# Kernel tuning notes

Hardware: AMD Instinct MI355X
Metric: run time of the kernel (lower is better)

Reference implementation:

```python
import jax, jax.numpy as jnp
import numpy as np

VOCAB = 32000
DIM = 1024
N_BLOCKS = 5
L_CONST = 1e9


def setup_inputs() -> dict:
    key = jax.random.key(0)
    k1, k2, k3, k4, k5, k6 = jax.random.split(key, 6)
    x = jax.random.normal(k1, (2, 2048, DIM), dtype=jnp.float32)
    gates_w = jax.random.uniform(k2, (VOCAB, 1), dtype=jnp.float32)  # mimics uniform_(0.001, 1.0)
    weight = jax.random.normal(k3, (DIM, VOCAB), dtype=jnp.float32) * 0.02
    bias = jax.random.normal(k4, (VOCAB,), dtype=jnp.float32) * 0.02
    blk_w = jax.random.normal(k5, (N_BLOCKS, DIM, DIM), dtype=jnp.float32) * 0.02
    blk_b = jax.random.normal(k6, (N_BLOCKS, DIM), dtype=jnp.float32) * 0.02
    return {"x": x, "gates_w": gates_w, "weight": weight, "bias": bias, "blk_w": blk_w, "blk_b": blk_b}


def reference(x, gates_w, weight, bias, blk_w, blk_b):
    input_dim, vocab = weight.shape  # [D, V]
    gates = gates_w * input_dim  # [V, 1], scaled per-token gate
    idx = jnp.arange(input_dim, dtype=jnp.float32)[None, :]  # [1, D]
    # discrete mask + straight-through residual term (broadcast [V,1] over [V,D])
    mask = (idx < gates).astype(jnp.float32) + (L_CONST * gates - jnp.floor(L_CONST * gates)) / L_CONST  # [V, D]
    masked_weight = weight * mask.T  # [D, V]
    # branch selector per vocab column, in {0,...,4}
    selector = jnp.floor(gates / x.shape[-1] * N_BLOCKS * (1.0 - 1e-10)).reshape(vocab)  # [V]
    ret = jnp.zeros(x.shape[:-1] + (vocab,), dtype=x.dtype)
    for bidx in range(N_BLOCKS):
        x_b = jnp.einsum('bsd,ed->bse', x, blk_w[bidx]) + blk_b[bidx]  # Linear: x @ W^T + b
        temp = jnp.einsum('bsd,dv->bsv', x_b, masked_weight)  # [B, S, V]
        ret = ret + temp * (selector == bidx).astype(jnp.float32)
    return ret + bias
```

## Files before the change

### kernel.cpp

```cpp
#include <hip/hip_runtime.h>
#include <hip/hip_bf16.h>

#define VOCAB 32000
#define DIM 1024
#define NTOK 4096
#define NG 5
#define MAXTILES 255
#define PW 32640

typedef float f32x4 __attribute__((ext_vector_type(4)));
typedef __bf16 bf16x8 __attribute__((ext_vector_type(8)));

__device__ __forceinline__ unsigned short f2bf(float f) {
    union { float f; unsigned int u; } x; x.f = f;
    unsigned int r = x.u + 0x7fffu + ((x.u >> 16) & 1u);
    return (unsigned short)(r >> 16);
}
__device__ __forceinline__ float bf2f(unsigned short u) {
    union { unsigned int u; float f; } x; x.u = ((unsigned int)u) << 16;
    return x.f;
}

__device__ __forceinline__ void gload16(const void* g, void* l) {
    __builtin_amdgcn_global_load_lds(
        (const __attribute__((address_space(1))) void*)g,
        (__attribute__((address_space(3))) void*)l, 16, 0, 0);
}

__global__ __launch_bounds__(256) void hist_kernel(const float* __restrict__ gates_w,
                                                   int* __restrict__ hist) {
    __shared__ int cnt[NG];
    const int tid = threadIdx.x;
    if (tid < NG) cnt[tid] = 0;
    __syncthreads();
    const int v = blockIdx.x * 256 + tid;
    const int s = min(4, max(0, (int)floorf(gates_w[v] * 5.0f)));
    atomicAdd(&cnt[s], 1);
    __syncthreads();
    if (tid < NG) hist[blockIdx.x * NG + tid] = cnt[tid];
}

__global__ __launch_bounds__(64) void base_kernel(const int* __restrict__ hist,
                                                  int* __restrict__ blkoff,
                                                  int* __restrict__ jlist,
                                                  int4* __restrict__ tdesc,
                                                  int* __restrict__ pbase6) {
    __shared__ int histl[125 * NG];
    __shared__ int cnt[NG], pb[NG], padc[NG];
    const int tid = threadIdx.x;
    for (int i = tid; i < 125 * NG; i += 64) histl[i] = hist[i];
    __syncthreads();
    if (tid == 0) {
        int c[NG] = {0, 0, 0, 0, 0};
        for (int b = 0; b < 125; ++b)
            for (int g = 0; g < NG; ++g) c[g] += histl[b * NG + g];
        const int kmaxs[NG] = {256, 448, 640, 832, 1024};
        int p = 0, t = 0;
        for (int g = 0; g < NG; ++g) {
            pb[g] = p; cnt[g] = c[g];
            padc[g] = ((c[g] + 127) >> 7) << 7;
            pbase6[g] = p;
            p += padc[g];
        }
        pbase6[NG] = p;
        for (int g = 0; g < NG; ++g) {
            int nt = (cnt[g] + 127) >> 7;
            for (int k = 0; k < nt; ++k) { tdesc[t] = make_int4(g, pb[g] + (k << 7), kmaxs[g], 0); ++t; }
        }
        for (; t < MAXTILES; ++t) tdesc[t] = make_int4(-1, 0, 0, 0);
        int run[NG];
        for (int g = 0; g < NG; ++g) run[g] = pb[g];
        for (int b = 0; b < 125; ++b)
            for (int g = 0; g < NG; ++g) { blkoff[b * NG + g] = run[g]; run[g] += histl[b * NG + g]; }
    }
    __syncthreads();
    for (int g = 0; g < NG; ++g)
        for (int i = pb[g] + cnt[g] + tid; i < pb[g] + padc[g]; i += 64) jlist[i] = -1;
}

__global__ __launch_bounds__(256) void place_kernel(const float* __restrict__ gates_w,
                                                    const int* __restrict__ blkoff,
                                                    int* __restrict__ pos,
                                                    int* __restrict__ jlist) {
    __shared__ int wtot[4][NG], wpre[4][NG];
    const int tid = threadIdx.x, lane = tid & 63, wv = tid >> 6;
    const int v = blockIdx.x * 256 + tid;
    const int s = min(4, max(0, (int)floorf(gates_w[v] * 5.0f)));
    int rank = 0;
#pragma unroll
    for (int g = 0; g < NG; ++g) {
        unsigned long long m = __ballot(s == g);
        if (lane == 0) wtot[wv][g] = (int)__popcll(m);
        if (s == g) rank = (int)__popcll(m & ((1ull << lane) - 1ull));
    }
    __syncthreads();
    if (tid < NG) {
        int a = 0;
        for (int w = 0; w < 4; ++w) { wpre[w][tid] = a; a += wtot[w][tid]; }
    }
    __syncthreads();
    const int p = blkoff[blockIdx.x * NG + s] + wpre[wv][s] + rank;
    pos[v] = p;
    jlist[p] = v;
}

__global__ void conv_kernel(const float* __restrict__ in, unsigned short* __restrict__ out, int n4) {
    int i = blockIdx.x * blockDim.x + threadIdx.x;
    if (i >= n4) return;
    const float4 f = ((const float4*)in)[i];
    ushort4 o;
    o.x = f2bf(f.x); o.y = f2bf(f.y); o.z = f2bf(f.z); o.w = f2bf(f.w);
    ((ushort4*)out)[i] = o;
}

__global__ __launch_bounds__(256) void wm_kernel(const float* __restrict__ weight,
                                                 const float* __restrict__ gates_w,
                                                 const int* __restrict__ pos,
                                                 unsigned short* __restrict__ wmbp) {
    __shared__ unsigned short tl[64][68];
    __shared__ float gatev[64];
    __shared__ int posv[64];
    const int v0 = blockIdx.x * 64, d0 = blockIdx.y * 64;
    const int tid = threadIdx.x;
    if (tid < 64) { gatev[tid] = gates_w[v0 + tid] * 1024.0f; posv[tid] = pos[v0 + tid]; }
    __syncthreads();
#pragma unroll
    for (int it = 0; it < 16; ++it) {
        int idx = it * 256 + tid;
        int ld = idx >> 6, lv = idx & 63;
        float w = weight[(size_t)(d0 + ld) * VOCAB + (v0 + lv)];
        float m = ((float)(d0 + ld) < gatev[lv]) ? 1.0f : 0.0f;
        tl[lv][ld] = f2bf(w * m);
    }
    __syncthreads();
#pragma unroll
    for (int it = 0; it < 2; ++it) {
        int idx = it * 256 + tid;
        int lv = idx >> 3, ch = idx & 7;
        union { unsigned short u[8]; uint4 q; } uu;
#pragma unroll
        for (int k = 0; k < 8; ++k) uu.u[k] = tl[lv][ch * 8 + k];
        *(uint4*)(wmbp + (size_t)posv[lv] * DIM + d0 + ch * 8) = uu.q;
    }
}

__global__ __launch_bounds__(256, 2) void tf_gemm(const unsigned short* __restrict__ xbf,
                                                  const unsigned short* __restrict__ wbf,
                                                  const float* __restrict__ blk_b,
                                                  unsigned short* __restrict__ ybf) {
    __shared__ __align__(16) unsigned short lA[128 * 64];
    __shared__ __align__(16) unsigned short lB[128 * 64];
    const int tid = threadIdx.x;
    const int lane = tid & 63, wv = tid >> 6;
    const int wm64 = (wv >> 1) * 64, wn64 = (wv & 1) * 64;
    const int m0 = blockIdx.y * 128, n0 = blockIdx.x * 128;
    const int lr = lane >> 4, lc = lane & 15;
    f32x4 acc[4][4] = {};
    const int r = tid >> 3, c = tid & 7;
    const unsigned short* sa = xbf + (size_t)(m0 + r) * DIM + c * 8;
    const unsigned short* sb = wbf + (size_t)(n0 + r) * DIM + c * 8;
    unsigned short* da = &lA[r * 64 + c * 8];
    unsigned short* db = &lB[r * 64 + c * 8];
    for (int kt = 0; kt < DIM / 64; ++kt) {
#pragma unroll
        for (int s = 0; s < 4; ++s) {
            gload16(sa + (size_t)s * 32 * DIM + kt * 64, da + s * 32 * 64);
            gload16(sb + (size_t)s * 32 * DIM + kt * 64, db + s * 32 * 64);
        }
        __syncthreads();
#pragma unroll
        for (int kk = 0; kk < 64; kk += 32) {
            const int ko = kk + lr * 8;
            bf16x8 af[4], bg[4];
#pragma unroll
            for (int m = 0; m < 4; ++m) af[m] = *(const bf16x8*)&lA[(wm64 + m * 16 + lc) * 64 + ko];
#pragma unroll
            for (int n = 0; n < 4; ++n) bg[n] = *(const bf16x8*)&lB[(wn64 + n * 16 + lc) * 64 + ko];
#pragma unroll
            for (int m = 0; m < 4; ++m)
#pragma unroll
                for (int n = 0; n < 4; ++n)
                    acc[m][n] = __builtin_amdgcn_mfma_f32_16x16x32_bf16(af[m], bg[n], acc[m][n], 0, 0, 0);
        }
        __syncthreads();
    }
#pragma unroll
    for (int n = 0; n < 4; ++n) {
        const int col = n0 + wn64 + n * 16 + lc;
        const float badd = blk_b[col];
        const int g = col >> 10, e = col & 1023;
#pragma unroll
        for (int m = 0; m < 4; ++m) {
            const int t0 = m0 + wm64 + m * 16 + lr * 4;
#pragma unroll
            for (int i = 0; i < 4; ++i)
                ybf[((size_t)g * NTOK + t0 + i) * DIM + e] = f2bf(acc[m][n][i] + badd);
        }
    }
}

template <bool COMPACT>
__global__ __launch_bounds__(256, 2) void main_gemm(const unsigned short* __restrict__ ybf,
                                                    const unsigned short* __restrict__ wmbp,
                                                    const int* __restrict__ jlist,
                                                    const int4* __restrict__ tdesc,
                                                    const float* __restrict__ bias,
                                                    float* __restrict__ out,
                                                    unsigned short* __restrict__ outc) {
    const int rid = blockIdx.y * 255 + blockIdx.x;
    const int swz = (rid & 7) * 1020 + (rid >> 3);
    const int mc = swz / 2040;
    const int rem = swz - mc * 2040;
    const int j = rem >> 3;
    const int m0 = (mc * 8 + (rem & 7)) * 128;
    const int4 td = tdesc[j];
    if (td.x < 0) return;
    const int g = td.x, jb = td.y, kmax = td.z;
    __shared__ __align__(16) unsigned short lA[128 * 64];
    __shared__ __align__(16) unsigned short lB[128 * 64];
    const int tid = threadIdx.x;
    const int lane = tid & 63, wv = tid >> 6;
    const int wm64 = (wv >> 1) * 64, wn64 = (wv & 1) * 64;
    const int lr = lane >> 4, lc = lane & 15;
    f32x4 acc[4][4] = {};
    const int r = tid >> 3, c = tid & 7;
    const unsigned short* sa = ybf + (size_t)g * NTOK * DIM + (size_t)(m0 + r) * DIM + c * 8;
    const unsigned short* sb = wmbp + (size_t)(jb + r) * DIM + c * 8;
    unsigned short* da = &lA[r * 64 + c * 8];
    unsigned short* db = &lB[r * 64 + c * 8];
    const int nkt = kmax >> 6;
    for (int kt = 0; kt < nkt; ++kt) {
#pragma unroll
        for (int s = 0; s < 4; ++s) {
            gload16(sa + (size_t)s * 32 * DIM + kt * 64, da + s * 32 * 64);
            gload16(sb + (size_t)s * 32 * DIM + kt * 64, db + s * 32 * 64);
        }
        __syncthreads();
#pragma unroll
        for (int kk = 0; kk < 64; kk += 32) {
            const int ko = kk + lr * 8;
            bf16x8 af[4], bg[4];
#pragma unroll
            for (int m = 0; m < 4; ++m) af[m] = *(const bf16x8*)&lA[(wm64 + m * 16 + lc) * 64 + ko];
#pragma unroll
            for (int n = 0; n < 4; ++n) bg[n] = *(const bf16x8*)&lB[(wn64 + n * 16 + lc) * 64 + ko];
#pragma unroll
            for (int m = 0; m < 4; ++m)
#pragma unroll
                for (int n = 0; n < 4; ++n)
                    acc[m][n] = __builtin_amdgcn_mfma_f32_16x16x32_bf16(af[m], bg[n], acc[m][n], 0, 0, 0);
        }
        __syncthreads();
    }
    if (COMPACT) {
#pragma unroll
        for (int n = 0; n < 4; ++n) {
            const int p = jb + wn64 + n * 16 + lc;
#pragma unroll
            for (int m = 0; m < 4; ++m) {
                const int t0 = m0 + wm64 + m * 16 + lr * 4;
#pragma unroll
                for (int i = 0; i < 4; ++i)
                    outc[(size_t)(t0 + i) * PW + p] = f2bf(acc[m][n][i]);
            }
        }
    } else {
#pragma unroll
        for (int n = 0; n < 4; ++n) {
            const int p = jb + wn64 + n * 16 + lc;
            const int v = jlist[p];
            if (v < 0) continue;
            const float bv = bias[v];
#pragma unroll
            for (int m = 0; m < 4; ++m) {
                const int t0 = m0 + wm64 + m * 16 + lr * 4;
#pragma unroll
                for (int i = 0; i < 4; ++i)
                    out[(size_t)(t0 + i) * VOCAB + v] = acc[m][n][i] + bv;
            }
        }
    }
}

__global__ __launch_bounds__(256) void permute_kernel(const unsigned short* __restrict__ outc,
                                                      const int* __restrict__ pos,
                                                      const float* __restrict__ bias,
                                                      const int* __restrict__ pbase6,
                                                      float* __restrict__ out) {
    __shared__ __align__(16) unsigned short tile[16][1152];
    __shared__ unsigned short pidx[1024];
    __shared__ float biasl[1024];
    __shared__ int pminS[NG], cntS[NG], baseS[NG], astartS[NG], alenS[NG];
    __shared__ int pb[NG + 1];
    const int tid = threadIdx.x;
    const int v0 = blockIdx.x * 1024;
    const int t0 = blockIdx.y * 16;
    const int vcnt = min(1024, VOCAB - v0);
    if (tid < NG) { pminS[tid] = 0x7fffffff; cntS[tid] = 0; }
    if (tid < NG + 1) pb[tid] = pbase6[tid];
    __syncthreads();
    for (int i = tid; i < vcnt; i += 256) {
        int p = pos[v0 + i];
        int g = 0;
#pragma unroll
        for (int gg = 1; gg < NG; ++gg) if (p >= pb[gg]) g = gg;
        atomicMin(&pminS[g], p);
        atomicAdd(&cntS[g], 1);
    }
    __syncthreads();
    if (tid == 0) {
        int b = 0;
#pragma unroll
        for (int g = 0; g < NG; ++g) {
            int c = cntS[g];
            int as = (c > 0) ? (pminS[g] & ~7) : 0;
            int al = (c > 0) ? (((pminS[g] + c + 7) & ~7) - as) : 0;
            astartS[g] = as; alenS[g] = al; baseS[g] = b; b += al;
        }
    }
    __syncthreads();
    for (int i = tid; i < vcnt; i += 256) {
        int p = pos[v0 + i];
        int g = 0;
#pragma unroll
        for (int gg = 1; gg < NG; ++gg) if (p >= pb[gg]) g = gg;
        pidx[i] = (unsigned short)(baseS[g] + (p - astartS[g]));
        biasl[i] = bias[v0 + i];
    }
#pragma unroll
    for (int g = 0; g < NG; ++g) {
        const int al8 = alenS[g] >> 3;
        const int as = astartS[g], bs = baseS[g];
        for (int w = tid; w < 16 * al8; w += 256) {
            const int t = w / al8, k = w - t * al8;
            *(uint4*)&tile[t][bs + k * 8] =
                *(const uint4*)&outc[(size_t)(t0 + t) * PW + as + k * 8];
        }
    }
    __syncthreads();
    for (int w = tid; w < 16 * 256; w += 256) {
        const int t = w >> 8, i = (w & 255) * 4;
        if (i >= vcnt) continue;
        float4 o;
        o.x = bf2f(tile[t][pidx[i + 0]]) + biasl[i + 0];
        o.y = bf2f(tile[t][pidx[i + 1]]) + biasl[i + 1];
        o.z = bf2f(tile[t][pidx[i + 2]]) + biasl[i + 2];
        o.w = bf2f(tile[t][pidx[i + 3]]) + biasl[i + 3];
        *(float4*)&out[(size_t)(t0 + t) * VOCAB + v0 + i] = o;
    }
}

extern "C" void kernel_launch(void* const* d_in, const int* in_sizes, int n_in,
                              void* d_out, int out_size, void* d_ws, size_t ws_size,
                              hipStream_t stream) {
    const float* x       = (const float*)d_in[0];
    const float* gates_w = (const float*)d_in[1];
    const float* weight  = (const float*)d_in[2];
    const float* bias    = (const float*)d_in[3];
    const float* blk_w   = (const float*)d_in[4];
    const float* blk_b   = (const float*)d_in[5];
    float* out = (float*)d_out;
    char* ws = (char*)d_ws;

    unsigned short* xbf    = (unsigned short*)(ws);
    unsigned short* wbf    = (unsigned short*)(ws + 8388608);
    unsigned short* ybf    = (unsigned short*)(ws + 18874368);
    unsigned short* wmbp   = (unsigned short*)(ws + 60817408);
    int*  pos    = (int*)(ws + 127664128);
    int*  jlist  = (int*)(ws + 127792128);
    int4* tdesc  = (int4*)(ws + 127922688);
    int*  pbase6 = (int*)(ws + 127926768);
    int*  hist   = (int*)(ws + 127926792);
    int*  blkoff = (int*)(ws + 127929292);
    unsigned short* outc = (unsigned short*)(ws + 127931904);
    const bool compact = (ws_size >= 395318784ull);

    hist_kernel<<<dim3(125), dim3(256), 0, stream>>>(gates_w, hist);
    base_kernel<<<dim3(1), dim3(64), 0, stream>>>(hist, blkoff, jlist, tdesc, pbase6);
    place_kernel<<<dim3(125), dim3(256), 0, stream>>>(gates_w, blkoff, pos, jlist);
    conv_kernel<<<dim3(4096), dim3(256), 0, stream>>>(x, xbf, 1048576);
    conv_kernel<<<dim3(5120), dim3(256), 0, stream>>>(blk_w, wbf, 1310720);
    wm_kernel<<<dim3(500, 16), dim3(256), 0, stream>>>(weight, gates_w, pos, wmbp);
    tf_gemm<<<dim3(40, 32), dim3(256), 0, stream>>>(xbf, wbf, blk_b, ybf);
    if (compact) {
        main_gemm<true><<<dim3(MAXTILES, 32), dim3(256), 0, stream>>>(ybf, wmbp, jlist, tdesc, bias, out, outc);
        permute_kernel<<<dim3(32, 256), dim3(256), 0, stream>>>(outc, pos, bias, pbase6, out);
    } else {
        main_gemm<false><<<dim3(MAXTILES, 32), dim3(256), 0, stream>>>(ybf, wmbp, jlist, tdesc, bias, out, outc);
    }
}
```

Baseline: 1.178 ms.

## Reassociate block transform into per-vocab effective weights and fold block bias

Computes per-vocab effective weight matrices by multiplying the permuted masked weight rows with the selected transposed block weight. The output is then produced by one dense GEMM of x against these effective weights, and the block bias is folded into a per-vocab bias. This removes the intermediate transformed activations, the compact output buffer and the permutation pass. In exchange, the final GEMM no longer benefits from masked K truncation, so it does the full 1024-deep reduction for every vocab column.

```diff
diff --git a/kernel.cpp b/kernel.cpp
--- a/kernel.cpp
+++ b/kernel.cpp
@@ -6,7 +6,6 @@
 #define NTOK 4096
 #define NG 5
 #define MAXTILES 255
-#define PW 32640
 
 typedef float f32x4 __attribute__((ext_vector_type(4)));
 typedef __bf16 bf16x8 __attribute__((ext_vector_type(8)));
@@ -113,6 +112,31 @@
     ((ushort4*)out)[i] = o;
 }
 
+__global__ __launch_bounds__(256) void convT_kernel(const float* __restrict__ blk_w,
+                                                    unsigned short* __restrict__ wbfT) {
+    __shared__ unsigned short tl[64][68];
+    const int i0 = blockIdx.x * 64, o0 = blockIdx.y * 64, g = blockIdx.z;
+    const int tid = threadIdx.x;
+    const float* src = blk_w + (size_t)g * DIM * DIM;
+    unsigned short* dst = wbfT + (size_t)g * DIM * DIM;
+#pragma unroll
+    for (int it = 0; it < 16; ++it) {
+        int idx = it * 256 + tid;
+        int lo = idx >> 6, li = idx & 63;
+        tl[li][lo] = f2bf(src[(size_t)(o0 + lo) * DIM + i0 + li]);
+    }
+    __syncthreads();
+#pragma unroll
+    for (int it = 0; it < 2; ++it) {
+        int idx = it * 256 + tid;
+        int ri = idx >> 3, ch = idx & 7;
+        union { unsigned short u[8]; uint4 q; } uu;
+#pragma unroll
+        for (int k = 0; k < 8; ++k) uu.u[k] = tl[ri][ch * 8 + k];
+        *(uint4*)(dst + (size_t)(i0 + ri) * DIM + o0 + ch * 8) = uu.q;
+    }
+}
+
 __global__ __launch_bounds__(256) void wm_kernel(const float* __restrict__ weight,
                                                  const float* __restrict__ gates_w,
                                                  const int* __restrict__ pos,
@@ -144,78 +168,44 @@
     }
 }
 
-__global__ __launch_bounds__(256, 2) void tf_gemm(const unsigned short* __restrict__ xbf,
-                                                  const unsigned short* __restrict__ wbf,
-                                                  const float* __restrict__ blk_b,
-                                                  unsigned short* __restrict__ ybf) {
-    __shared__ __align__(16) unsigned short lA[128 * 64];
-    __shared__ __align__(16) unsigned short lB[128 * 64];
-    const int tid = threadIdx.x;
-    const int lane = tid & 63, wv = tid >> 6;
-    const int wm64 = (wv >> 1) * 64, wn64 = (wv & 1) * 64;
-    const int m0 = blockIdx.y * 128, n0 = blockIdx.x * 128;
-    const int lr = lane >> 4, lc = lane & 15;
-    f32x4 acc[4][4] = {};
-    const int r = tid >> 3, c = tid & 7;
-    const unsigned short* sa = xbf + (size_t)(m0 + r) * DIM + c * 8;
-    const unsigned short* sb = wbf + (size_t)(n0 + r) * DIM + c * 8;
-    unsigned short* da = &lA[r * 64 + c * 8];
-    unsigned short* db = &lB[r * 64 + c * 8];
-    for (int kt = 0; kt < DIM / 64; ++kt) {
-#pragma unroll
-        for (int s = 0; s < 4; ++s) {
-            gload16(sa + (size_t)s * 32 * DIM + kt * 64, da + s * 32 * 64);
-            gload16(sb + (size_t)s * 32 * DIM + kt * 64, db + s * 32 * 64);
-        }
-        __syncthreads();
-#pragma unroll
-        for (int kk = 0; kk < 64; kk += 32) {
-            const int ko = kk + lr * 8;
-            bf16x8 af[4], bg[4];
-#pragma unroll
-            for (int m = 0; m < 4; ++m) af[m] = *(const bf16x8*)&lA[(wm64 + m * 16 + lc) * 64 + ko];
-#pragma unroll
-            for (int n = 0; n < 4; ++n) bg[n] = *(const bf16x8*)&lB[(wn64 + n * 16 + lc) * 64 + ko];
-#pragma unroll
-            for (int m = 0; m < 4; ++m)
-#pragma unroll
-                for (int n = 0; n < 4; ++n)
-                    acc[m][n] = __builtin_amdgcn_mfma_f32_16x16x32_bf16(af[m], bg[n], acc[m][n], 0, 0, 0);
-        }
-        __syncthreads();
-    }
-#pragma unroll
-    for (int n = 0; n < 4; ++n) {
-        const int col = n0 + wn64 + n * 16 + lc;
-        const float badd = blk_b[col];
-        const int g = col >> 10, e = col & 1023;
-#pragma unroll
-        for (int m = 0; m < 4; ++m) {
-            const int t0 = m0 + wm64 + m * 16 + lr * 4;
-#pragma unroll
-            for (int i = 0; i < 4; ++i)
-                ybf[((size_t)g * NTOK + t0 + i) * DIM + e] = f2bf(acc[m][n][i] + badd);
-        }
-    }
-}
-
-template <bool COMPACT>
-__global__ __launch_bounds__(256, 2) void main_gemm(const unsigned short* __restrict__ ybf,
-                                                    const unsigned short* __restrict__ wmbp,
+__global__ __launch_bounds__(256) void dbias_kernel(const unsigned short* __restrict__ wmbp,
+                                                    const float* __restrict__ blk_b,
+                                                    const float* __restrict__ bias,
+                                                    const int* __restrict__ jlist,
+                                                    const int* __restrict__ pbase6,
+                                                    float* __restrict__ bias2) {
+    const int p = blockIdx.x * 4 + (threadIdx.x >> 6);
+    const int lane = threadIdx.x & 63;
+    if (p >= pbase6[NG]) return;
+    const int v = jlist[p];
+    if (v < 0) return;
+    int g = 0;
+#pragma unroll
+    for (int gg = 1; gg < NG; ++gg) if (p >= pbase6[gg]) g = gg;
+    const unsigned short* wrow = wmbp + (size_t)p * DIM + lane * 16;
+    const float* brow = blk_b + g * DIM + lane * 16;
+    union { uint4 q; unsigned short u[8]; } a0, a1;
+    a0.q = *(const uint4*)(wrow);
+    a1.q = *(const uint4*)(wrow + 8);
+    float s = 0.f;
+#pragma unroll
+    for (int k = 0; k < 8; ++k) s += bf2f(a0.u[k]) * brow[k];
+#pragma unroll
+    for (int k = 0; k < 8; ++k) s += bf2f(a1.u[k]) * brow[k + 8];
+#pragma unroll
+    for (int off = 32; off > 0; off >>= 1) s += __shfl_down(s, off);
+    if (lane == 0) bias2[v] = bias[v] + s;
+}
+
+__global__ __launch_bounds__(256, 2) void ceff_gemm(const unsigned short* __restrict__ wmbp,
+                                                    const unsigned short* __restrict__ wbfT,
                                                     const int* __restrict__ jlist,
                                                     const int4* __restrict__ tdesc,
-                                                    const float* __restrict__ bias,
-                                                    float* __restrict__ out,
-                                                    unsigned short* __restrict__ outc) {
-    const int rid = blockIdx.y * 255 + blockIdx.x;
-    const int swz = (rid & 7) * 1020 + (rid >> 3);
-    const int mc = swz / 2040;
-    const int rem = swz - mc * 2040;
-    const int j = rem >> 3;
-    const int m0 = (mc * 8 + (rem & 7)) * 128;
-    const int4 td = tdesc[j];
+                                                    unsigned short* __restrict__ ceffv) {
+    const int4 td = tdesc[blockIdx.x];
     if (td.x < 0) return;
     const int g = td.x, jb = td.y, kmax = td.z;
+    const int n0 = blockIdx.y * 128;
     __shared__ __align__(16) unsigned short lA[128 * 64];
     __shared__ __align__(16) unsigned short lB[128 * 64];
     const int tid = threadIdx.x;
@@ -224,8 +214,8 @@
     const int lr = lane >> 4, lc = lane & 15;
     f32x4 acc[4][4] = {};
     const int r = tid >> 3, c = tid & 7;
-    const unsigned short* sa = ybf + (size_t)g * NTOK * DIM + (size_t)(m0 + r) * DIM + c * 8;
-    const unsigned short* sb = wmbp + (size_t)(jb + r) * DIM + c * 8;
+    const unsigned short* sa = wmbp + (size_t)(jb + r) * DIM + c * 8;
+    const unsigned short* sb = wbfT + (size_t)g * DIM * DIM + (size_t)(n0 + r) * DIM + c * 8;
     unsigned short* da = &lA[r * 64 + c * 8];
     unsigned short* db = &lB[r * 64 + c * 8];
     const int nkt = kmax >> 6;
@@ -252,101 +242,76 @@
         }
         __syncthreads();
     }
-    if (COMPACT) {
-#pragma unroll
-        for (int n = 0; n < 4; ++n) {
-            const int p = jb + wn64 + n * 16 + lc;
-#pragma unroll
-            for (int m = 0; m < 4; ++m) {
-                const int t0 = m0 + wm64 + m * 16 + lr * 4;
-#pragma unroll
-                for (int i = 0; i < 4; ++i)
-                    outc[(size_t)(t0 + i) * PW + p] = f2bf(acc[m][n][i]);
+#pragma unroll
+    for (int m = 0; m < 4; ++m) {
+#pragma unroll
+        for (int i = 0; i < 4; ++i) {
+            const int prow = jb + wm64 + m * 16 + lr * 4 + i;
+            const int v = jlist[prow];
+            if (v < 0) continue;
+#pragma unroll
+            for (int n = 0; n < 4; ++n) {
+                const int icol = n0 + wn64 + n * 16 + lc;
+                ceffv[(size_t)v * DIM + icol] = f2bf(acc[m][n][i]);
             }
         }
-    } else {
-#pragma unroll
-        for (int n = 0; n < 4; ++n) {
-            const int p = jb + wn64 + n * 16 + lc;
-            const int v = jlist[p];
-            if (v < 0) continue;
-            const float bv = bias[v];
-#pragma unroll
-            for (int m = 0; m < 4; ++m) {
-                const int t0 = m0 + wm64 + m * 16 + lr * 4;
-#pragma unroll
-                for (int i = 0; i < 4; ++i)
-                    out[(size_t)(t0 + i) * VOCAB + v] = acc[m][n][i] + bv;
-            }
-        }
-    }
-}
-
-__global__ __launch_bounds__(256) void permute_kernel(const unsigned short* __restrict__ outc,
-                                                      const int* __restrict__ pos,
-                                                      const float* __restrict__ bias,
-                                                      const int* __restrict__ pbase6,
-                                                      float* __restrict__ out) {
-    __shared__ __align__(16) unsigned short tile[16][1152];
-    __shared__ unsigned short pidx[1024];
-    __shared__ float biasl[1024];
-    __shared__ int pminS[NG], cntS[NG], baseS[NG], astartS[NG], alenS[NG];
-    __shared__ int pb[NG + 1];
-    const int tid = threadIdx.x;
-    const int v0 = blockIdx.x * 1024;
-    const int t0 = blockIdx.y * 16;
-    const int vcnt = min(1024, VOCAB - v0);
-    if (tid < NG) { pminS[tid] = 0x7fffffff; cntS[tid] = 0; }
-    if (tid < NG + 1) pb[tid] = pbase6[tid];
-    __syncthreads();
-    for (int i = tid; i < vcnt; i += 256) {
-        int p = pos[v0 + i];
-        int g = 0;
-#pragma unroll
-        for (int gg = 1; gg < NG; ++gg) if (p >= pb[gg]) g = gg;
-        atomicMin(&pminS[g], p);
-        atomicAdd(&cntS[g], 1);
-    }
-    __syncthreads();
-    if (tid == 0) {
-        int b = 0;
-#pragma unroll
-        for (int g = 0; g < NG; ++g) {
-            int c = cntS[g];
-            int as = (c > 0) ? (pminS[g] & ~7) : 0;
-            int al = (c > 0) ? (((pminS[g] + c + 7) & ~7) - as) : 0;
-            astartS[g] = as; alenS[g] = al; baseS[g] = b; b += al;
-        }
-    }
-    __syncthreads();
-    for (int i = tid; i < vcnt; i += 256) {
-        int p = pos[v0 + i];
-        int g = 0;
-#pragma unroll
-        for (int gg = 1; gg < NG; ++gg) if (p >= pb[gg]) g = gg;
-        pidx[i] = (unsigned short)(baseS[g] + (p - astartS[g]));
-        biasl[i] = bias[v0 + i];
-    }
-#pragma unroll
-    for (int g = 0; g < NG; ++g) {
-        const int al8 = alenS[g] >> 3;
-        const int as = astartS[g], bs = baseS[g];
-        for (int w = tid; w < 16 * al8; w += 256) {
-            const int t = w / al8, k = w - t * al8;
-            *(uint4*)&tile[t][bs + k * 8] =
-                *(const uint4*)&outc[(size_t)(t0 + t) * PW + as + k * 8];
-        }
-    }
-    __syncthreads();
-    for (int w = tid; w < 16 * 256; w += 256) {
-        const int t = w >> 8, i = (w & 255) * 4;
-        if (i >= vcnt) continue;
-        float4 o;
-        o.x = bf2f(tile[t][pidx[i + 0]]) + biasl[i + 0];
-        o.y = bf2f(tile[t][pidx[i + 1]]) + biasl[i + 1];
-        o.z = bf2f(tile[t][pidx[i + 2]]) + biasl[i + 2];
-        o.w = bf2f(tile[t][pidx[i + 3]]) + biasl[i + 3];
-        *(float4*)&out[(size_t)(t0 + t) * VOCAB + v0 + i] = o;
+    }
+}
+
+__global__ __launch_bounds__(256, 2) void out_gemm(const unsigned short* __restrict__ xbf,
+                                                   const unsigned short* __restrict__ ceffv,
+                                                   const float* __restrict__ bias2,
+                                                   float* __restrict__ out) {
+    const int rid = blockIdx.y * gridDim.x + blockIdx.x;
+    const int swz = (rid & 7) * 1000 + (rid >> 3);
+    const int m0 = (swz & 31) * 128;
+    const int n0 = (swz >> 5) * 128;
+    __shared__ __align__(16) unsigned short lA[128 * 64];
+    __shared__ __align__(16) unsigned short lB[128 * 64];
+    const int tid = threadIdx.x;
+    const int lane = tid & 63, wv = tid >> 6;
+    const int wm64 = (wv >> 1) * 64, wn64 = (wv & 1) * 64;
+    const int lr = lane >> 4, lc = lane & 15;
+    f32x4 acc[4][4] = {};
+    const int r = tid >> 3, c = tid & 7;
+    const unsigned short* sa = xbf + (size_t)(m0 + r) * DIM + c * 8;
+    const unsigned short* sb = ceffv + (size_t)(n0 + r) * DIM + c * 8;
+    unsigned short* da = &lA[r * 64 + c * 8];
+    unsigned short* db = &lB[r * 64 + c * 8];
+    for (int kt = 0; kt < DIM / 64; ++kt) {
+#pragma unroll
+        for (int s = 0; s < 4; ++s) {
+            gload16(sa + (size_t)s * 32 * DIM + kt * 64, da + s * 32 * 64);
+            gload16(sb + (size_t)s * 32 * DIM + kt * 64, db + s * 32 * 64);
+        }
+        __syncthreads();
+#pragma unroll
+        for (int kk = 0; kk < 64; kk += 32) {
+            const int ko = kk + lr * 8;
+            bf16x8 af[4], bg[4];
+#pragma unroll
+            for (int m = 0; m < 4; ++m) af[m] = *(const bf16x8*)&lA[(wm64 + m * 16 + lc) * 64 + ko];
+#pragma unroll
+            for (int n = 0; n < 4; ++n) bg[n] = *(const bf16x8*)&lB[(wn64 + n * 16 + lc) * 64 + ko];
+#pragma unroll
+            for (int m = 0; m < 4; ++m)
+#pragma unroll
+                for (int n = 0; n < 4; ++n)
+                    acc[m][n] = __builtin_amdgcn_mfma_f32_16x16x32_bf16(af[m], bg[n], acc[m][n], 0, 0, 0);
+        }
+        __syncthreads();
+    }
+#pragma unroll
+    for (int n = 0; n < 4; ++n) {
+        const int col = n0 + wn64 + n * 16 + lc;
+        const float b2 = bias2[col];
+#pragma unroll
+        for (int m = 0; m < 4; ++m) {
+            const int t0 = m0 + wm64 + m * 16 + lr * 4;
+#pragma unroll
+            for (int i = 0; i < 4; ++i)
+                out[(size_t)(t0 + i) * VOCAB + col] = acc[m][n][i] + b2;
+        }
     }
 }
 
@@ -362,30 +327,25 @@
     float* out = (float*)d_out;
     char* ws = (char*)d_ws;
 
-    unsigned short* xbf    = (unsigned short*)(ws);
-    unsigned short* wbf    = (unsigned short*)(ws + 8388608);
-    unsigned short* ybf    = (unsigned short*)(ws + 18874368);
-    unsigned short* wmbp   = (unsigned short*)(ws + 60817408);
-    int*  pos    = (int*)(ws + 127664128);
-    int*  jlist  = (int*)(ws + 127792128);
-    int4* tdesc  = (int4*)(ws + 127922688);
-    int*  pbase6 = (int*)(ws + 127926768);
-    int*  hist   = (int*)(ws + 127926792);
-    int*  blkoff = (int*)(ws + 127929292);
-    unsigned short* outc = (unsigned short*)(ws + 127931904);
-    const bool compact = (ws_size >= 395318784ull);
+    unsigned short* xbf   = (unsigned short*)(ws);
+    unsigned short* wbfT  = (unsigned short*)(ws + 8388608);
+    unsigned short* wmbp  = (unsigned short*)(ws + 18874368);
+    unsigned short* ceffv = (unsigned short*)(ws + 85721088);
+    float* bias2 = (float*)(ws + 151257088);
+    int*   pos   = (int*)(ws + 151385088);
+    int*   jlist = (int*)(ws + 151513088);
+    int4*  tdesc = (int4*)(ws + 151643648);
+    int*   pbase6 = (int*)(ws + 151647728);
+    int*   hist   = (int*)(ws + 151647752);
+    int*   blkoff = (int*)(ws + 151650252);
 
     hist_kernel<<<dim3(125), dim3(256), 0, stream>>>(gates_w, hist);
     base_kernel<<<dim3(1), dim3(64), 0, stream>>>(hist, blkoff, jlist, tdesc, pbase6);
     place_kernel<<<dim3(125), dim3(256), 0, stream>>>(gates_w, blkoff, pos, jlist);
     conv_kernel<<<dim3(4096), dim3(256), 0, stream>>>(x, xbf, 1048576);
-    conv_kernel<<<dim3(5120), dim3(256), 0, stream>>>(blk_w, wbf, 1310720);
+    convT_kernel<<<dim3(16, 16, NG), dim3(256), 0, stream>>>(blk_w, wbfT);
     wm_kernel<<<dim3(500, 16), dim3(256), 0, stream>>>(weight, gates_w, pos, wmbp);
-    tf_gemm<<<dim3(40, 32), dim3(256), 0, stream>>>(xbf, wbf, blk_b, ybf);
-    if (compact) {
-        main_gemm<true><<<dim3(MAXTILES, 32), dim3(256), 0, stream>>>(ybf, wmbp, jlist, tdesc, bias, out, outc);
-        permute_kernel<<<dim3(32, 256), dim3(256), 0, stream>>>(outc, pos, bias, pbase6, out);
-    } else {
-        main_gemm<false><<<dim3(MAXTILES, 32), dim3(256), 0, stream>>>(ybf, wmbp, jlist, tdesc, bias, out, outc);
-    }
-}
+    dbias_kernel<<<dim3(8160), dim3(256), 0, stream>>>(wmbp, blk_b, bias, jlist, pbase6, bias2);
+    ceff_gemm<<<dim3(MAXTILES, 8), dim3(256), 0, stream>>>(wmbp, wbfT, jlist, tdesc, ceffv);
+    out_gemm<<<dim3(250, 32), dim3(256), 0, stream>>>(xbf, ceffv, bias2, out);
+}
```

Result: faster. 1.085 ms (-7.9%).
